# Kernel tuning notes

Measured on AMD Instinct MI355X. Metric: run time of the kernel, lower is better.

## Reference

```python
import jax, jax.numpy as jnp
import numpy as np

HEADS = 8

def _pos_enc(n, channels, dtype):
    # PositionalEncoding1D: interleaved sin/cos over node index
    inv_freq = 1.0 / (10000.0 ** (jnp.arange(0, channels, 2, dtype=jnp.float32) / channels))
    sinp = jnp.arange(n, dtype=jnp.float32)[:, None] * inv_freq[None, :]  # [n, channels//2]
    emb = jnp.stack((jnp.sin(sinp), jnp.cos(sinp)), axis=-1).reshape(n, channels)
    return emb.astype(dtype)

def _transformer_conv(x, src, dst, Wq, bq, Wk, bk, Wv, bv, Ws, bs):
    # PyG TransformerConv (concat=True, root_weight=True, eval -> no dropout)
    n = x.shape[0]
    hc = Wq.shape[1]
    c = hc // HEADS
    q = (x @ Wq + bq).reshape(n, HEADS, c)
    k = (x @ Wk + bk).reshape(n, HEADS, c)
    v = (x @ Wv + bv).reshape(n, HEADS, c)
    # per-edge attention logits, softmax grouped by target node
    logits = jnp.einsum('ehc,ehc->eh', q[dst], k[src]) / jnp.sqrt(jnp.asarray(c, x.dtype))
    m = jax.ops.segment_max(logits, dst, num_segments=n)
    e = jnp.exp(logits - m[dst])
    denom = jax.ops.segment_sum(e, dst, num_segments=n)
    alpha = e / denom[dst]  # [E, H]
    out = jax.ops.segment_sum(alpha[:, :, None] * v[src], dst, num_segments=n)
    return out.reshape(n, hc) + x @ Ws + bs

def _gcn_conv(x, src, dst, W, b):
    # PyG GCNConv: add self-loops, symmetric normalization, linear (no bias) then bias
    n = x.shape[0]
    loop = jnp.arange(n, dtype=src.dtype)
    s = jnp.concatenate([src, loop])
    d = jnp.concatenate([dst, loop])
    deg = jax.ops.segment_sum(jnp.ones(s.shape[0], x.dtype), d, num_segments=n)
    dis = jax.lax.rsqrt(jnp.maximum(deg, jnp.asarray(1.0, x.dtype)))
    norm = dis[s] * dis[d]  # [E+N]
    xw = x @ W
    return jax.ops.segment_sum(norm[:, None] * xw[s], d, num_segments=n) + b

def _forward(x, edge_index, W_embed, b_embed,
             Wq1, bq1, Wk1, bk1, Wv1, bv1, Ws1, bs1, Wh1, bh1,
             Wq2, bq2, Wk2, bk2, Wv2, bv2, Ws2, bs2, Wh2, bh2,
             Wg3, bg3, Wg4, bg4):
    src, dst = edge_index[0], edge_index[1]
    h = x @ W_embed + b_embed                       # [N, H1]
    h = h + _pos_enc(h.shape[0], h.shape[1], h.dtype)
    h = _transformer_conv(h, src, dst, Wq1, bq1, Wk1, bk1, Wv1, bv1, Ws1, bs1)
    h = h @ Wh1 + bh1
    h = _transformer_conv(h, src, dst, Wq2, bq2, Wk2, bk2, Wv2, bv2, Ws2, bs2)
    h = h @ Wh2 + bh2
    h = _gcn_conv(h, src, dst, Wg3, bg3)            # dropout is eval no-op
    h = _gcn_conv(h, src, dst, Wg4, bg4)
    return h[None]                                  # [1, N, OUT]

def setup_inputs() -> dict:
    N, E, IN, H1, H2, H3, OUT = 50000, 400000, 63, 32, 32, 32, 32
    HC = HEADS * H2
    key = jax.random.key(0)
    ks = jax.random.split(key, 32)
    p = lambda k, shp: (jax.random.normal(k, shp, dtype=jnp.float32) * 0.02)
    inp = {
        'x': jax.random.normal(ks[0], (N, IN), dtype=jnp.float32),
        'edge_index': jax.random.randint(ks[1], (2, E), 0, N, dtype=jnp.int64 if jax.config.jax_enable_x64 else jnp.int32),
        'W_embed': p(ks[2], (IN, H1)), 'b_embed': p(ks[3], (H1,)),
        'Wq1': p(ks[4], (H1, HC)), 'bq1': p(ks[5], (HC,)),
        'Wk1': p(ks[6], (H1, HC)), 'bk1': p(ks[7], (HC,)),
        'Wv1': p(ks[8], (H1, HC)), 'bv1': p(ks[9], (HC,)),
        'Ws1': p(ks[10], (H1, HC)), 'bs1': p(ks[11], (HC,)),
        'Wh1': p(ks[12], (HC, H1)), 'bh1': p(ks[13], (H1,)),
        'Wq2': p(ks[14], (H1, HC)), 'bq2': p(ks[15], (HC,)),
        'Wk2': p(ks[16], (H1, HC)), 'bk2': p(ks[17], (HC,)),
        'Wv2': p(ks[18], (H1, HC)), 'bv2': p(ks[19], (HC,)),
        'Ws2': p(ks[20], (H1, HC)), 'bs2': p(ks[21], (HC,)),
        'Wh2': p(ks[22], (HC, H1)), 'bh2': p(ks[23], (H1,)),
        'Wg3': p(ks[24], (H2, H3)), 'bg3': p(ks[25], (H3,)),
        'Wg4': p(ks[26], (H3, OUT)), 'bg4': p(ks[27], (OUT,)),
    }
    return inp

def reference(x, edge_index, W_embed, b_embed,
              Wq1, bq1, Wk1, bk1, Wv1, bv1, Ws1, bs1, Wh1, bh1,
              Wq2, bq2, Wk2, bk2, Wv2, bv2, Ws2, bs2, Wh2, bh2,
              Wg3, bg3, Wg4, bg4):
    return _forward(x, edge_index, W_embed, b_embed,
                    Wq1, bq1, Wk1, bk1, Wv1, bv1, Ws1, bs1, Wh1, bh1,
                    Wq2, bq2, Wk2, bk2, Wv2, bv2, Ws2, bs2, Wh2, bh2,
                    Wg3, bg3, Wg4, bg4)
```

## Files before the change

kernel.cpp:

```cpp
#include <hip/hip_runtime.h>
#include <cstddef>


#define NH 8
#define HCH 256
#define D32 32
#define INCH 63
#define CSCALE 0.25503485356f

__device__ __forceinline__ unsigned short f2bf(float f) {
    unsigned u = __float_as_uint(f);
    u += 0x7fff + ((u >> 16) & 1);
    return (unsigned short)(u >> 16);
}
__device__ __forceinline__ float bfu(unsigned short u) {
    return __uint_as_float(((unsigned)u) << 16);
}

__device__ const float c_invf[16] = {
    1.0f, 0.5623413251903491f, 0.31622776601683794f, 0.17782794100389228f,
    0.1f, 0.05623413251903491f, 0.031622776601683791f, 0.017782794100389228f,
    0.01f, 0.005623413251903491f, 0.0031622776601683794f, 0.0017782794100389228f,
    0.001f, 0.0005623413251903491f, 0.00031622776601683794f, 0.00017782794100389227f
};

__global__ __launch_bounds__(256) void k_embed(
    const float* __restrict__ x, const float* __restrict__ W,
    const float* __restrict__ b, float* __restrict__ H, int N, int nbMain,
    int E, const int* __restrict__ dst, int* __restrict__ cnt,
    const float* __restrict__ Wsk1, const float* __restrict__ bsk1,
    const float* __restrict__ Wh1,  const float* __restrict__ bh1,
    const float* __restrict__ Wsk2, const float* __restrict__ bsk2,
    const float* __restrict__ Wh2,  const float* __restrict__ bh2,
    float* __restrict__ WCB)
{
    if (blockIdx.x >= nbMain + 2) {
        int e = (blockIdx.x - nbMain - 2) * 256 + threadIdx.x;
        if (e < E) atomicAdd(&cnt[dst[e]], 1);
        return;
    }
    if (blockIdx.x >= nbMain) {
        int lay = blockIdx.x - nbMain;
        const float* Wsk = lay ? Wsk2 : Wsk1;
        const float* bsk = lay ? bsk2 : bsk1;
        const float* Wh  = lay ? Wh2  : Wh1;
        const float* bh  = lay ? bh2  : bh1;
        float* o = WCB + lay * 1056;
        for (int i = threadIdx.x; i < D32 * D32 + D32; i += 256) {
            if (i < D32 * D32) {
                int r = i >> 5, c = i & 31;
                float a = 0.f;
                for (int k = 0; k < HCH; ++k) a = fmaf(Wsk[r * HCH + k], Wh[k * D32 + c], a);
                o[i] = a;
            } else {
                int c = i - D32 * D32;
                float a = bh[c];
                for (int k = 0; k < HCH; ++k) a = fmaf(bsk[k], Wh[k * D32 + c], a);
                o[1024 + c] = a;
            }
        }
        return;
    }
    __shared__ float xs[8][64];
    __shared__ float ws[INCH * D32];
    int row0 = blockIdx.x * 8;
    for (int i = threadIdx.x; i < INCH * D32; i += 256) ws[i] = W[i];
    for (int i = threadIdx.x; i < 8 * INCH; i += 256) {
        int r = i / INCH, cc = i % INCH;
        int gr = row0 + r;
        xs[r][cc] = (gr < N) ? x[(size_t)gr * INCH + cc] : 0.f;
    }
    __syncthreads();
    int lr = threadIdx.x >> 5, c = threadIdx.x & 31;
    int row = row0 + lr;
    if (row >= N) return;
    float acc = b[c];
#pragma unroll
    for (int k = 0; k < INCH; ++k) acc = fmaf(xs[lr][k], ws[k * D32 + c], acc);
    float phase = (float)row * c_invf[c >> 1];
    float pe = (c & 1) ? cosf(phase) : sinf(phase);
    H[(size_t)row * D32 + c] = acc + pe;
}

__global__ void k_scan1(const int* __restrict__ cnt, int* __restrict__ rowptr,
                        int* __restrict__ partials, float* __restrict__ DIS, int N)
{
    __shared__ int s[256];
    int g = blockIdx.x * 256 + threadIdx.x;
    int myc = (g < N) ? cnt[g] : 0;
    if (g < N) DIS[g] = rsqrtf((float)myc + 1.0f);
    s[threadIdx.x] = myc;
    __syncthreads();
    for (int off = 1; off < 256; off <<= 1) {
        int t = (threadIdx.x >= off) ? s[threadIdx.x - off] : 0;
        __syncthreads();
        s[threadIdx.x] += t;
        __syncthreads();
    }
    if (g < N) rowptr[g + 1] = s[threadIdx.x];
    if (threadIdx.x == 255) partials[blockIdx.x] = s[255];
}
__global__ void k_scan2(int* __restrict__ partials, int nb) {
    __shared__ int s[256];
    int t = threadIdx.x;
    s[t] = (t < nb) ? partials[t] : 0;
    __syncthreads();
    for (int off = 1; off < 256; off <<= 1) {
        int v = (t >= off) ? s[t - off] : 0;
        __syncthreads();
        s[t] += v;
        __syncthreads();
    }
    partials[t] = (t == 0) ? 0 : s[t - 1];
}
__global__ void k_scan3b(int* __restrict__ rowptr, const int* __restrict__ partials,
                         int* __restrict__ cur, int N)
{
    int g = blockIdx.x * 256 + threadIdx.x;
    int add = partials[blockIdx.x];
    int oldprev = 0;
    if (g < N && threadIdx.x > 0) oldprev = rowptr[g];
    __syncthreads();
    if (g < N) {
        rowptr[g + 1] += add;
        cur[g] = (threadIdx.x == 0) ? add : oldprev + add;
        if (g == 0) rowptr[0] = 0;
    }
}
__global__ void k_fill(const int* __restrict__ src, const int* __restrict__ dst,
                       int* __restrict__ cur, int* __restrict__ colsrc, int E)
{
    int e = blockIdx.x * 256 + threadIdx.x;
    if (e < E) {
        int p = atomicAdd(&cur[dst[e]], 1);
        colsrc[p] = src[e];
    }
}

__global__ __launch_bounds__(256) void k_h32_to_kvqs(
    const float* __restrict__ Hm,
    const float* __restrict__ Wq, const float* __restrict__ bq,
    const float* __restrict__ Wk, const float* __restrict__ bk,
    const float* __restrict__ Wv, const float* __restrict__ bv,
    const float* __restrict__ WCBl,
    unsigned short* __restrict__ Qb, unsigned short* __restrict__ KV,
    float* __restrict__ SKIP, int N)
{
    __shared__ float hs[8][33];
    int row0 = blockIdx.x * 8;
    int c = threadIdx.x;
    {
        int r = threadIdx.x >> 5, k = threadIdx.x & 31;
        int gr = row0 + r;
        hs[r][k] = (gr < N) ? Hm[(size_t)gr * D32 + k] : 0.f;
    }
    __syncthreads();
    float aQ[8], aK[8], aV[8], aS[8];
    float bQ = bq[c], bK = bk[c], bV = bv[c];
    float bS = (c < 32) ? WCBl[1024 + c] : 0.f;
#pragma unroll
    for (int r = 0; r < 8; ++r) { aQ[r] = bQ; aK[r] = bK; aV[r] = bV; aS[r] = bS; }
#pragma unroll 8
    for (int k = 0; k < 32; ++k) {
        float wq = Wq[k * HCH + c], wk = Wk[k * HCH + c], wv = Wv[k * HCH + c];
        float wc = (c < 32) ? WCBl[k * D32 + c] : 0.f;
#pragma unroll
        for (int r = 0; r < 8; ++r) {
            float h = hs[r][k];
            aQ[r] = fmaf(h, wq, aQ[r]);
            aK[r] = fmaf(h, wk, aK[r]);
            aV[r] = fmaf(h, wv, aV[r]);
            aS[r] = fmaf(h, wc, aS[r]);
        }
    }
    int hh = c >> 5, cc = c & 31, ss = cc >> 2, ii = cc & 3;
#pragma unroll
    for (int r = 0; r < 8; ++r) {
        int gr = row0 + r;
        if (gr < N) {
            Qb[(size_t)gr * HCH + c] = f2bf(aQ[r] * CSCALE);
            size_t kb = (size_t)gr * 512 + hh * 64 + ss * 8 + ii;
            KV[kb]     = f2bf(aK[r]);
            KV[kb + 4] = f2bf(aV[r]);
            if (c < 32) SKIP[(size_t)gr * D32 + c] = aS[r];
        }
    }
}

#define PROC(A, PIDX)                                                        \
    {                                                                        \
        float t1, t;                                                         \
        asm("v_dot2_f32_bf16 %0, %1, %2, %3"                                 \
            : "=v"(t1) : "v"(A.y), "v"(qy), "v"(zf));                        \
        asm("v_dot2_f32_bf16 %0, %1, %2, %3"                                 \
            : "=v"(t) : "v"(A.x), "v"(qx), "v"(t1));                         \
        t += __shfl_xor(t, 1, 64);                                           \
        t += __shfl_xor(t, 2, 64);                                           \
        t += __shfl_xor(t, 4, 64);                                           \
        float wg = ((PIDX) <= pl) ? __builtin_amdgcn_exp2f(t) : 0.f;         \
        l += wg;                                                             \
        acc0 = fmaf(wg, __uint_as_float(A.z << 16), acc0);                   \
        acc1 = fmaf(wg, __uint_as_float(A.z & 0xffff0000u), acc1);           \
        acc2 = fmaf(wg, __uint_as_float(A.w << 16), acc2);                   \
        acc3 = fmaf(wg, __uint_as_float(A.w & 0xffff0000u), acc3);           \
    }
#define CLD(B, I) colsrc[min((B) + (I), pl)]

__global__ __launch_bounds__(256) void k_attn(
    const uint4* __restrict__ KV4, const uint2* __restrict__ Qb2,
    const float* __restrict__ SKIP, float* __restrict__ H,
    const int* __restrict__ rowptr, const int* __restrict__ colsrc,
    const float* __restrict__ Wh, int N)
{
    __shared__ float os[4][264];
    int w = threadIdx.x >> 6, lane = threadIdx.x & 63;
    int d = blockIdx.x * 4 + w;
    bool act = d < N;

    unsigned qx = 0u, qy = 0u;
    if (act) {
        uint2 qw = Qb2[(size_t)d * 64 + lane];
        qx = qw.x; qy = qw.y;
    }
    float zf = 0.f;

    float l = 0.f, acc0 = 0.f, acc1 = 0.f, acc2 = 0.f, acc3 = 0.f;
    if (act) {
        int p0 = rowptr[d], p1 = rowptr[d + 1];
        if (p1 > p0) {
            int pl = p1 - 1;
            int s0 = CLD(p0, 0), s1 = CLD(p0, 1), s2 = CLD(p0, 2), s3 = CLD(p0, 3);
            uint4 A0 = KV4[(size_t)s0 * 64 + lane];
            uint4 A1 = KV4[(size_t)s1 * 64 + lane];
            uint4 A2 = KV4[(size_t)s2 * 64 + lane];
            uint4 A3 = KV4[(size_t)s3 * 64 + lane];
#pragma unroll 2
            for (int base = p0; base < p1; base += 4) {
                int nb2 = base + 4;
                int t0 = CLD(nb2, 0), t1c = CLD(nb2, 1), t2c = CLD(nb2, 2), t3c = CLD(nb2, 3);
                uint4 B0 = KV4[(size_t)t0 * 64 + lane];
                uint4 B1 = KV4[(size_t)t1c * 64 + lane];
                uint4 B2 = KV4[(size_t)t2c * 64 + lane];
                uint4 B3 = KV4[(size_t)t3c * 64 + lane];
                PROC(A0, base)
                PROC(A1, base + 1)
                PROC(A2, base + 2)
                PROC(A3, base + 3)
                A0 = B0; A1 = B1; A2 = B2; A3 = B3;
            }
        }
        float inv = (l > 0.f) ? 1.f / l : 0.f;
        int gch = (lane >> 3) * 32 + (lane & 7) * 4;
        os[w][gch + 0] = acc0 * inv;
        os[w][gch + 1] = acc1 * inv;
        os[w][gch + 2] = acc2 * inv;
        os[w][gch + 3] = acc3 * inv;
    }
    __syncthreads();

    if (act) {
        int c = lane & 31, half = lane >> 5;
        float a2 = half ? 0.f : SKIP[(size_t)d * D32 + c];
        int kb = half * 128;
#pragma unroll 8
        for (int kk = 0; kk < 128; ++kk)
            a2 = fmaf(os[w][kb + kk], Wh[(kb + kk) * D32 + c], a2);
        a2 += __shfl_xor(a2, 32, 64);
        if (lane < 32) H[(size_t)d * D32 + c] = a2;
    }
}

__global__ __launch_bounds__(256) void k_xw3(
    const float* __restrict__ X, const float* __restrict__ W,
    const float* __restrict__ DIS, unsigned short* __restrict__ O, int N)
{
    __shared__ float xs[8][33];
    __shared__ float ws[D32 * D32];
    int row0 = blockIdx.x * 8;
    int c = threadIdx.x & 31, lr = threadIdx.x >> 5;
    for (int i = threadIdx.x; i < D32 * D32; i += 256) ws[i] = W[i];
    {
        int gr = row0 + lr;
        xs[lr][c] = (gr < N) ? X[(size_t)gr * D32 + c] : 0.f;
    }
    __syncthreads();
    int row = row0 + lr;
    if (row >= N) return;
    float acc = 0.f;
#pragma unroll
    for (int k = 0; k < D32; ++k) acc = fmaf(xs[lr][k], ws[k * D32 + c], acc);
    O[(size_t)row * D32 + c] = f2bf(DIS[row] * acc);
}

__global__ __launch_bounds__(256) void k_gcn_f(
    const unsigned short* __restrict__ XWp, const float* __restrict__ DIS,
    const int* __restrict__ rowptr, const int* __restrict__ colsrc,
    const float* __restrict__ bg, const float* __restrict__ Wg4,
    unsigned short* __restrict__ XWout, int N)
{
    __shared__ float wgs[1024];
    for (int i = threadIdx.x; i < 1024; i += 256) wgs[i] = Wg4[i];
    __syncthreads();
    int g = threadIdx.x >> 5;
    int c = threadIdx.x & 31;
    int d = blockIdx.x * 8 + g;
    bool act = d < N;
    float dd = 0.f, h3 = 0.f;
    if (act) {
        float acc = bfu(XWp[(size_t)d * D32 + c]);
        int p0 = rowptr[d], p1 = rowptr[d + 1];
        if (p1 > p0) {
            int pl = p1 - 1;
            unsigned short uA = XWp[(size_t)CLD(p0, 0) * D32 + c];
            unsigned short uB = XWp[(size_t)CLD(p0, 1) * D32 + c];
            unsigned short uC = XWp[(size_t)CLD(p0, 2) * D32 + c];
            unsigned short uD = XWp[(size_t)CLD(p0, 3) * D32 + c];
#pragma unroll 4
            for (int p = p0; p < p1; ++p) {
                unsigned short uN = XWp[(size_t)CLD(p, 4) * D32 + c];
                acc += bfu(uA);
                uA = uB; uB = uC; uC = uD; uD = uN;
            }
        }
        dd = DIS[d];
        h3 = dd * acc + bg[c];
    }
    float s = 0.f;
#pragma unroll
    for (int k = 0; k < 32; ++k)
        s = fmaf(__shfl(h3, k, 32), wgs[k * D32 + c], s);
    if (act) XWout[(size_t)d * D32 + c] = f2bf(dd * s);
}

__global__ __launch_bounds__(256) void k_gcn_last(
    const unsigned short* __restrict__ XWp, const float* __restrict__ DIS,
    const int* __restrict__ rowptr, const int* __restrict__ colsrc,
    const float* __restrict__ bg, float* __restrict__ Out, int N)
{
    int g = threadIdx.x >> 5;
    int c = threadIdx.x & 31;
    int d = blockIdx.x * 8 + g;
    if (d >= N) return;
    float acc = bfu(XWp[(size_t)d * D32 + c]);
    int p0 = rowptr[d], p1 = rowptr[d + 1];
    if (p1 > p0) {
        int pl = p1 - 1;
        unsigned short uA = XWp[(size_t)CLD(p0, 0) * D32 + c];
        unsigned short uB = XWp[(size_t)CLD(p0, 1) * D32 + c];
        unsigned short uC = XWp[(size_t)CLD(p0, 2) * D32 + c];
        unsigned short uD = XWp[(size_t)CLD(p0, 3) * D32 + c];
#pragma unroll 4
        for (int p = p0; p < p1; ++p) {
            unsigned short uN = XWp[(size_t)CLD(p, 4) * D32 + c];
            acc += bfu(uA);
            uA = uB; uB = uC; uC = uD; uD = uN;
        }
    }
    Out[(size_t)d * D32 + c] = DIS[d] * acc + bg[c];
}

extern "C" void kernel_launch(void* const* d_in, const int* in_sizes, int n_in,
                              void* d_out, int out_size, void* d_ws, size_t ws_size,
                              hipStream_t stream)
{
    const float* x  = (const float*)d_in[0];
    const int*   ei = (const int*)d_in[1];
    const int N = in_sizes[0] / INCH;
    const int E = in_sizes[1] / 2;
    const int* src = ei;
    const int* dst = ei + E;

    const float* W_embed = (const float*)d_in[2];
    const float* b_embed = (const float*)d_in[3];
    const float* Wg3 = (const float*)d_in[24];
    const float* bg3 = (const float*)d_in[25];
    const float* Wg4 = (const float*)d_in[26];
    const float* bg4 = (const float*)d_in[27];

    unsigned short* KV  = (unsigned short*)d_ws;
    unsigned short* Qb  = KV + (size_t)N * 512;
    float* H      = (float*)(Qb + (size_t)N * HCH);
    float* SKIP   = H + (size_t)N * D32;
    unsigned short* XW1 = (unsigned short*)(SKIP + (size_t)N * D32);
    unsigned short* XW2 = XW1 + (size_t)N * D32;
    int*   rowptr = (int*)(XW2 + (size_t)N * D32);
    int*   colsrc = rowptr + (N + 1);
    int*   cursor = colsrc + E;
    int*   partials = cursor + N;
    float* DIS    = (float*)(partials + 256);
    float* WCB    = DIS + N;
    float* out    = (float*)d_out;

    const int nb8 = (N + 7) / 8;
    const int nb4 = (N + 3) / 4;
    const int nbN = (N + 255) / 256;
    const int nbE = (E + 255) / 256;

    hipMemsetAsync(cursor, 0, (size_t)N * sizeof(int), stream);

    k_embed<<<nb8 + 2 + nbE, 256, 0, stream>>>(
        x, W_embed, b_embed, H, N, nb8, E, dst, cursor,
        (const float*)d_in[10], (const float*)d_in[11],
        (const float*)d_in[12], (const float*)d_in[13],
        (const float*)d_in[20], (const float*)d_in[21],
        (const float*)d_in[22], (const float*)d_in[23], WCB);

    k_scan1<<<nbN, 256, 0, stream>>>(cursor, rowptr, partials, DIS, N);
    k_scan2<<<1, 256, 0, stream>>>(partials, nbN);
    k_scan3b<<<nbN, 256, 0, stream>>>(rowptr, partials, cursor, N);
    k_fill<<<nbE, 256, 0, stream>>>(src, dst, cursor, colsrc, E);

    for (int layer = 0; layer < 2; ++layer) {
        int base = 4 + layer * 10;
        const float* Wq = (const float*)d_in[base + 0];
        const float* bq = (const float*)d_in[base + 1];
        const float* Wk = (const float*)d_in[base + 2];
        const float* bk = (const float*)d_in[base + 3];
        const float* Wv = (const float*)d_in[base + 4];
        const float* bv = (const float*)d_in[base + 5];
        const float* Wh = (const float*)d_in[base + 8];

        k_h32_to_kvqs<<<nb8, 256, 0, stream>>>(
            H, Wq, bq, Wk, bk, Wv, bv, WCB + layer * 1056, Qb, KV, SKIP, N);
        k_attn<<<nb4, 256, 0, stream>>>(
            (const uint4*)KV, (const uint2*)Qb, SKIP, H, rowptr, colsrc, Wh, N);
    }

    k_xw3<<<nb8, 256, 0, stream>>>(H, Wg3, DIS, XW1, N);
    k_gcn_f<<<nb8, 256, 0, stream>>>(XW1, DIS, rowptr, colsrc, bg3, Wg4, XW2, N);
    k_gcn_last<<<nb8, 256, 0, stream>>>(XW2, DIS, rowptr, colsrc, bg4, out, N);
}
```

Measured before the change: 431.9 us.

## Pre-pack weights to bf16 pairs and use dot2 in QKV and output projections

Adds extra blocks to the embed kernel that repack the Q/K/V, output-projection and combined skip weights into packed bf16 pairs. The QKV projection and the attention output projection then use v_dot2_f32_bf16 on packed activations and weights, which halves the FMA count and the weight bytes loaded. The scan is also trimmed from three kernels to two by having each block reduce the preceding block partials itself. This lowers the precision of the hidden activations and weights to bf16 in these projections, which costs some accuracy.

```diff
diff --git a/kernel.cpp b/kernel.cpp
--- a/kernel.cpp
+++ b/kernel.cpp
@@ -16,6 +16,11 @@
 __device__ __forceinline__ float bfu(unsigned short u) {
     return __uint_as_float(((unsigned)u) << 16);
 }
+__device__ __forceinline__ unsigned packbf(float lo, float hi) {
+    return (unsigned)f2bf(lo) | ((unsigned)f2bf(hi) << 16);
+}
+#define DOT2(acc, a, b) \
+    asm("v_dot2_f32_bf16 %0, %1, %2, %0" : "+v"(acc) : "v"(a), "v"(b))
 
 __device__ const float c_invf[16] = {
     1.0f, 0.5623413251903491f, 0.31622776601683794f, 0.17782794100389228f,
@@ -32,11 +37,32 @@
     const float* __restrict__ Wh1,  const float* __restrict__ bh1,
     const float* __restrict__ Wsk2, const float* __restrict__ bsk2,
     const float* __restrict__ Wh2,  const float* __restrict__ bh2,
-    float* __restrict__ WCB)
-{
+    const float* __restrict__ Wq1, const float* __restrict__ Wk1,
+    const float* __restrict__ Wv1,
+    const float* __restrict__ Wq2, const float* __restrict__ Wk2,
+    const float* __restrict__ Wv2,
+    float* __restrict__ WCB,
+    unsigned* __restrict__ WQP, unsigned* __restrict__ WKP,
+    unsigned* __restrict__ WVP, unsigned* __restrict__ WHP,
+    unsigned* __restrict__ WCP)
+{
+    if (blockIdx.x >= nbMain + 10) {
+        int e = (blockIdx.x - nbMain - 10) * 256 + threadIdx.x;
+        if (e < E) atomicAdd(&cnt[dst[e]], 1);
+        return;
+    }
     if (blockIdx.x >= nbMain + 2) {
-        int e = (blockIdx.x - nbMain - 2) * 256 + threadIdx.x;
-        if (e < E) atomicAdd(&cnt[dst[e]], 1);
+        int p = blockIdx.x - nbMain - 2;
+        int lay = p >> 2, m = p & 3;
+        const float* Ws; unsigned* dp; int k2n, nc;
+        if (m == 0)      { Ws = lay ? Wq2 : Wq1; dp = WQP + lay * 4096; k2n = 16;  nc = 256; }
+        else if (m == 1) { Ws = lay ? Wk2 : Wk1; dp = WKP + lay * 4096; k2n = 16;  nc = 256; }
+        else if (m == 2) { Ws = lay ? Wv2 : Wv1; dp = WVP + lay * 4096; k2n = 16;  nc = 256; }
+        else             { Ws = lay ? Wh2 : Wh1; dp = WHP + lay * 4096; k2n = 128; nc = 32;  }
+        for (int i = threadIdx.x; i < k2n * nc; i += 256) {
+            int k2 = i / nc, c = i % nc;
+            dp[i] = packbf(Ws[(2 * k2) * nc + c], Ws[(2 * k2 + 1) * nc + c]);
+        }
         return;
     }
     if (blockIdx.x >= nbMain) {
@@ -59,6 +85,11 @@
                 o[1024 + c] = a;
             }
         }
+        __syncthreads();
+        for (int i = threadIdx.x; i < 512; i += 256) {
+            int k2 = i >> 5, c = i & 31;
+            WCP[lay * 512 + i] = packbf(o[(2 * k2) * 32 + c], o[(2 * k2 + 1) * 32 + c]);
+        }
         return;
     }
     __shared__ float xs[8][64];
@@ -100,30 +131,25 @@
     if (g < N) rowptr[g + 1] = s[threadIdx.x];
     if (threadIdx.x == 255) partials[blockIdx.x] = s[255];
 }
-__global__ void k_scan2(int* __restrict__ partials, int nb) {
+__global__ void k_scan3b(int* __restrict__ rowptr, const int* __restrict__ partials,
+                         int* __restrict__ cur, int N, int nb)
+{
     __shared__ int s[256];
     int t = threadIdx.x;
-    s[t] = (t < nb) ? partials[t] : 0;
-    __syncthreads();
-    for (int off = 1; off < 256; off <<= 1) {
-        int v = (t >= off) ? s[t - off] : 0;
+    s[t] = (t < nb && t < (int)blockIdx.x) ? partials[t] : 0;
+    __syncthreads();
+    for (int off = 128; off > 0; off >>= 1) {
+        if (t < off) s[t] += s[t + off];
         __syncthreads();
-        s[t] += v;
-        __syncthreads();
-    }
-    partials[t] = (t == 0) ? 0 : s[t - 1];
-}
-__global__ void k_scan3b(int* __restrict__ rowptr, const int* __restrict__ partials,
-                         int* __restrict__ cur, int N)
-{
-    int g = blockIdx.x * 256 + threadIdx.x;
-    int add = partials[blockIdx.x];
+    }
+    int add = s[0];
+    int g = blockIdx.x * 256 + t;
     int oldprev = 0;
-    if (g < N && threadIdx.x > 0) oldprev = rowptr[g];
+    if (g < N && t > 0) oldprev = rowptr[g];
     __syncthreads();
     if (g < N) {
         rowptr[g + 1] += add;
-        cur[g] = (threadIdx.x == 0) ? add : oldprev + add;
+        cur[g] = (t == 0) ? add : oldprev + add;
         if (g == 0) rowptr[0] = 0;
     }
 }
@@ -139,20 +165,22 @@
 
 __global__ __launch_bounds__(256) void k_h32_to_kvqs(
     const float* __restrict__ Hm,
-    const float* __restrict__ Wq, const float* __restrict__ bq,
-    const float* __restrict__ Wk, const float* __restrict__ bk,
-    const float* __restrict__ Wv, const float* __restrict__ bv,
-    const float* __restrict__ WCBl,
+    const unsigned* __restrict__ WqP, const float* __restrict__ bq,
+    const unsigned* __restrict__ WkP, const float* __restrict__ bk,
+    const unsigned* __restrict__ WvP, const float* __restrict__ bv,
+    const unsigned* __restrict__ WcP, const float* __restrict__ WCBl,
     unsigned short* __restrict__ Qb, unsigned short* __restrict__ KV,
     float* __restrict__ SKIP, int N)
 {
-    __shared__ float hs[8][33];
+    __shared__ unsigned hp[8][17];
     int row0 = blockIdx.x * 8;
     int c = threadIdx.x;
-    {
-        int r = threadIdx.x >> 5, k = threadIdx.x & 31;
+    if (threadIdx.x < 128) {
+        int r = threadIdx.x >> 4, k2 = threadIdx.x & 15;
         int gr = row0 + r;
-        hs[r][k] = (gr < N) ? Hm[(size_t)gr * D32 + k] : 0.f;
+        float2 hv = (gr < N) ? ((const float2*)Hm)[(size_t)gr * 16 + k2]
+                             : make_float2(0.f, 0.f);
+        hp[r][k2] = packbf(hv.x, hv.y);
     }
     __syncthreads();
     float aQ[8], aK[8], aV[8], aS[8];
@@ -160,17 +188,19 @@
     float bS = (c < 32) ? WCBl[1024 + c] : 0.f;
 #pragma unroll
     for (int r = 0; r < 8; ++r) { aQ[r] = bQ; aK[r] = bK; aV[r] = bV; aS[r] = bS; }
-#pragma unroll 8
-    for (int k = 0; k < 32; ++k) {
-        float wq = Wq[k * HCH + c], wk = Wk[k * HCH + c], wv = Wv[k * HCH + c];
-        float wc = (c < 32) ? WCBl[k * D32 + c] : 0.f;
+#pragma unroll 4
+    for (int k2 = 0; k2 < 16; ++k2) {
+        unsigned wq = WqP[k2 * 256 + c];
+        unsigned wk = WkP[k2 * 256 + c];
+        unsigned wv = WvP[k2 * 256 + c];
+        unsigned wc = (c < 32) ? WcP[k2 * 32 + c] : 0u;
 #pragma unroll
         for (int r = 0; r < 8; ++r) {
-            float h = hs[r][k];
-            aQ[r] = fmaf(h, wq, aQ[r]);
-            aK[r] = fmaf(h, wk, aK[r]);
-            aV[r] = fmaf(h, wv, aV[r]);
-            aS[r] = fmaf(h, wc, aS[r]);
+            unsigned h = hp[r][k2];
+            DOT2(aQ[r], h, wq);
+            DOT2(aK[r], h, wk);
+            DOT2(aV[r], h, wv);
+            DOT2(aS[r], h, wc);
         }
     }
     int hh = c >> 5, cc = c & 31, ss = cc >> 2, ii = cc & 3;
@@ -210,9 +240,9 @@
     const uint4* __restrict__ KV4, const uint2* __restrict__ Qb2,
     const float* __restrict__ SKIP, float* __restrict__ H,
     const int* __restrict__ rowptr, const int* __restrict__ colsrc,
-    const float* __restrict__ Wh, int N)
-{
-    __shared__ float os[4][264];
+    const unsigned* __restrict__ WhP, int N)
+{
+    __shared__ unsigned osp[4][136];
     int w = threadIdx.x >> 6, lane = threadIdx.x & 63;
     int d = blockIdx.x * 4 + w;
     bool act = d < N;
@@ -250,21 +280,22 @@
             }
         }
         float inv = (l > 0.f) ? 1.f / l : 0.f;
-        int gch = (lane >> 3) * 32 + (lane & 7) * 4;
-        os[w][gch + 0] = acc0 * inv;
-        os[w][gch + 1] = acc1 * inv;
-        os[w][gch + 2] = acc2 * inv;
-        os[w][gch + 3] = acc3 * inv;
+        int g2 = (lane >> 3) * 16 + (lane & 7) * 2;
+        osp[w][g2]     = packbf(acc0 * inv, acc1 * inv);
+        osp[w][g2 + 1] = packbf(acc2 * inv, acc3 * inv);
     }
     __syncthreads();
 
     if (act) {
         int c = lane & 31, half = lane >> 5;
         float a2 = half ? 0.f : SKIP[(size_t)d * D32 + c];
-        int kb = half * 128;
+        int kb2 = half * 64;
 #pragma unroll 8
-        for (int kk = 0; kk < 128; ++kk)
-            a2 = fmaf(os[w][kb + kk], Wh[(kb + kk) * D32 + c], a2);
+        for (int kk = 0; kk < 64; ++kk) {
+            unsigned o = osp[w][kb2 + kk];
+            unsigned wh = WhP[(kb2 + kk) * 32 + c];
+            DOT2(a2, o, wh);
+        }
         a2 += __shfl_xor(a2, 32, 64);
         if (lane < 32) H[(size_t)d * D32 + c] = a2;
     }
@@ -389,6 +420,11 @@
     int*   partials = cursor + N;
     float* DIS    = (float*)(partials + 256);
     float* WCB    = DIS + N;
+    unsigned* WQP = (unsigned*)(WCB + 2 * 1056);
+    unsigned* WKP = WQP + 2 * 4096;
+    unsigned* WVP = WKP + 2 * 4096;
+    unsigned* WHP = WVP + 2 * 4096;
+    unsigned* WCP = WHP + 2 * 4096;
     float* out    = (float*)d_out;
 
     const int nb8 = (N + 7) / 8;
@@ -398,32 +434,36 @@
 
     hipMemsetAsync(cursor, 0, (size_t)N * sizeof(int), stream);
 
-    k_embed<<<nb8 + 2 + nbE, 256, 0, stream>>>(
+    k_embed<<<nb8 + 10 + nbE, 256, 0, stream>>>(
         x, W_embed, b_embed, H, N, nb8, E, dst, cursor,
         (const float*)d_in[10], (const float*)d_in[11],
         (const float*)d_in[12], (const float*)d_in[13],
         (const float*)d_in[20], (const float*)d_in[21],
-        (const float*)d_in[22], (const float*)d_in[23], WCB);
+        (const float*)d_in[22], (const float*)d_in[23],
+        (const float*)d_in[4],  (const float*)d_in[6],  (const float*)d_in[8],
+        (const float*)d_in[14], (const float*)d_in[16], (const float*)d_in[18],
+        WCB, WQP, WKP, WVP, WHP, WCP);
 
     k_scan1<<<nbN, 256, 0, stream>>>(cursor, rowptr, partials, DIS, N);
-    k_scan2<<<1, 256, 0, stream>>>(partials, nbN);
-    k_scan3b<<<nbN, 256, 0, stream>>>(rowptr, partials, cursor, N);
+    k_scan3b<<<nbN, 256, 0, stream>>>(rowptr, partials, cursor, N, nbN);
     k_fill<<<nbE, 256, 0, stream>>>(src, dst, cursor, colsrc, E);
 
     for (int layer = 0; layer < 2; ++layer) {
         int base = 4 + layer * 10;
-        const float* Wq = (const float*)d_in[base + 0];
         const float* bq = (const float*)d_in[base + 1];
-        const float* Wk = (const float*)d_in[base + 2];
         const float* bk = (const float*)d_in[base + 3];
-        const float* Wv = (const float*)d_in[base + 4];
         const float* bv = (const float*)d_in[base + 5];
-        const float* Wh = (const float*)d_in[base + 8];
 
         k_h32_to_kvqs<<<nb8, 256, 0, stream>>>(
-            H, Wq, bq, Wk, bk, Wv, bv, WCB + layer * 1056, Qb, KV, SKIP, N);
+            H,
+            WQP + layer * 4096, bq,
+            WKP + layer * 4096, bk,
+            WVP + layer * 4096, bv,
+            WCP + layer * 512, WCB + layer * 1056,
+            Qb, KV, SKIP, N);
         k_attn<<<nb4, 256, 0, stream>>>(
-            (const uint4*)KV, (const uint2*)Qb, SKIP, H, rowptr, colsrc, Wh, N);
+            (const uint4*)KV, (const uint2*)Qb, SKIP, H, rowptr, colsrc,
+            WHP + layer * 4096, N);
     }
 
     k_xw3<<<nb8, 256, 0, stream>>>(H, Wg3, DIS, XW1, N);
```

After: 368.2 us. 14.7% less time.
